# Performance work log

Measured on AMD Instinct MI355X. Metric: run time of the kernel, lower is better.

## Reference

```python
import jax, jax.numpy as jnp
import numpy as np

B, T, E, D = 4, 4096, 1024, 64

def setup_inputs() -> dict:
    key = jax.random.key(0)
    kx, kq, kk, kv = jax.random.split(key, 4)
    # kaiming_normal_ on [E, D] (fan_in = E in torch default mode='fan_in'):
    std = (2.0 / E) ** 0.5
    return {
        "x": jax.random.normal(kx, (B, T, E), dtype=jnp.float32),
        "Wq": jax.random.normal(kq, (E, D), dtype=jnp.float32) * std,
        "Wk": jax.random.normal(kk, (E, D), dtype=jnp.float32) * std,
        "Wv": jax.random.normal(kv, (E, D), dtype=jnp.float32) * std,
    }

def reference(x, Wq, Wk, Wv):
    q = jnp.einsum('bte,ei->bti', x, Wq)
    k = jnp.einsum('bte,ei->bti', x, Wk)
    v = jnp.einsum('bte,ei->bti', x, Wv)
    scale = 1.0 / jnp.sqrt(jnp.asarray(q.shape[-1], q.dtype))
    qk = jnp.einsum('bti,bTi->btT', q, k)  # [B, T, T] full score matrix
    s = jax.nn.softmax(qk * scale, axis=-1)
    return jnp.einsum('btT,bTi->bti', s, v)
```

## Files before the change

kernel.cpp:

```cpp
#include <hip/hip_runtime.h>
#include <stdint.h>


#define T_DIM 4096
#define E_DIM 1024
#define D_DIM 64
#define NROWS 16384

typedef __bf16 bf16x8 __attribute__((ext_vector_type(8)));
typedef float  f32x4  __attribute__((ext_vector_type(4)));

__global__ void conv_w(const float* __restrict__ Wq, const float* __restrict__ Wk,
                       const float* __restrict__ Wv, __bf16* __restrict__ wF)
{
    int idx = blockIdx.x * 256 + threadIdx.x;
    if (idx >= 196608) return;
    int j    = idx & 7;
    int lane = (idx >> 3) & 63;
    int n    = (idx >> 9) & 3;
    int ktG  = (idx >> 11) & 31;
    int m    = idx >> 16;
    int d = n * 16 + (lane & 15);
    int e = ktG * 32 + (lane >> 4) * 8 + j;
    const float* W = (m == 0) ? Wq : (m == 1) ? Wk : Wv;
    float v = W[e * D_DIM + d];
    if (m == 0) v *= 0.125f;
    wF[idx] = (__bf16)v;
}

__global__ __launch_bounds__(256) void aaaa_qkvpj(const float* __restrict__ x,
        const __bf16* __restrict__ wF,
        __bf16* __restrict__ Qp, __bf16* __restrict__ Kp, __bf16* __restrict__ Vt)
{
    __shared__ float red[12 * 16 * 66];

    const int tid  = threadIdx.x;
    const int lane = tid & 63;
    const int w    = tid >> 6;
    const int lrow = lane & 15;
    const int lq   = lane >> 4;
    const int r0   = blockIdx.x * 16;

    f32x4 acc[3][4] = {};
    const float* xrow = x + (long)(r0 + lrow) * E_DIM + w * 256;
    const __bf16* wl  = wF + lane * 8;

    #pragma unroll
    for (int kt = 0; kt < 8; ++kt) {
        const int k0 = kt * 32 + lq * 8;
        f32x4 xa = *(const f32x4*)(xrow + k0);
        f32x4 xb = *(const f32x4*)(xrow + k0 + 4);
        bf16x8 a;
        a[0] = (__bf16)xa[0]; a[1] = (__bf16)xa[1];
        a[2] = (__bf16)xa[2]; a[3] = (__bf16)xa[3];
        a[4] = (__bf16)xb[0]; a[5] = (__bf16)xb[1];
        a[6] = (__bf16)xb[2]; a[7] = (__bf16)xb[3];
        #pragma unroll
        for (int m = 0; m < 3; ++m) {
            #pragma unroll
            for (int n = 0; n < 4; ++n) {
                bf16x8 b = *(const bf16x8*)(wl + (((((m * 32) + (w * 8) + kt) * 4) + n) << 9));
                acc[m][n] = __builtin_amdgcn_mfma_f32_16x16x32_bf16(a, b, acc[m][n], 0, 0, 0);
            }
        }
    }

    #pragma unroll
    for (int m = 0; m < 3; ++m)
        #pragma unroll
        for (int n = 0; n < 4; ++n)
            #pragma unroll
            for (int j = 0; j < 4; ++j)
                red[((w * 3 + m) * 16 + lq * 4 + j) * 66 + n * 16 + lrow] = acc[m][n][j];
    __syncthreads();

    const long gb = r0 >> 12;
    const int  t0 = r0 & 4095;

    #pragma unroll
    for (int m = 0; m < 2; ++m)
        #pragma unroll
        for (int e = 0; e < 4; ++e) {
            int idx = e * 256 + tid;
            int r = idx >> 6, c = idx & 63;
            float s = red[(m * 16 + r) * 66 + c] + red[((3 + m) * 16 + r) * 66 + c]
                    + red[((6 + m) * 16 + r) * 66 + c] + red[((9 + m) * 16 + r) * 66 + c];
            (m == 0 ? Qp : Kp)[(long)(r0 + r) * D_DIM + c] = (__bf16)s;
        }
    #pragma unroll
    for (int e = 0; e < 4; ++e) {
        int idx = e * 256 + tid;
        int d = idx >> 4, tr = idx & 15;
        float s = red[(2 * 16 + tr) * 66 + d] + red[(5 * 16 + tr) * 66 + d]
                + red[(8 * 16 + tr) * 66 + d] + red[(11 * 16 + tr) * 66 + d];
        Vt[gb * (D_DIM * (long)T_DIM) + (long)d * T_DIM + t0 + tr] = (__bf16)s;
    }
}

#define PADK 72
__global__ __launch_bounds__(256) void flash_attn(const __bf16* __restrict__ Qp,
        const __bf16* __restrict__ Kp, const __bf16* __restrict__ Vt,
        float* __restrict__ Op, float* __restrict__ mp, float* __restrict__ lp,
        float* __restrict__ out, int ntile, int direct)
{
    __shared__ __bf16 kt[64][PADK];
    __shared__ __bf16 vt[64][PADK];
    __shared__ __bf16 pl[4][16][PADK];

    const int tid  = threadIdx.x;
    const int lane = tid & 63;
    const int w    = tid >> 6;
    const int lrow = lane & 15;
    const int lq   = lane >> 4;
    const int bid  = blockIdx.x;
    const int sp   = bid >> 8;
    const int rem  = bid & 255;
    const int b    = rem >> 6;
    const int qt   = rem & 63;
    const long base = (long)b * T_DIM;

    bf16x8 qf[2];
    {
        const __bf16* qptr = Qp + (base + qt * 64 + w * 16 + lrow) * D_DIM + lq * 8;
        qf[0] = *(const bf16x8*)(qptr);
        qf[1] = *(const bf16x8*)(qptr + 32);
    }

    f32x4 oacc[4] = {};
    float mrun[4], lrun[4];
    #pragma unroll
    for (int j = 0; j < 4; ++j) { mrun[j] = -1e30f; lrun[j] = 0.f; }

    const int ldrow = tid >> 2;
    const int ldcol = (tid & 3) * 16;
    const __bf16* vbase = Vt + b * (D_DIM * (long)T_DIM) + (long)ldrow * T_DIM;

    const int kv0 = sp * ntile;
    #pragma unroll 1
    for (int kv = kv0; kv < kv0 + ntile; ++kv) {
        __syncthreads();
        {
            const __bf16* kg = Kp + (base + kv * 64 + ldrow) * D_DIM + ldcol;
            const __bf16* vg = vbase + kv * 64 + ldcol;
            bf16x8 k0 = *(const bf16x8*)kg;
            bf16x8 k1 = *(const bf16x8*)(kg + 8);
            bf16x8 v0 = *(const bf16x8*)vg;
            bf16x8 v1 = *(const bf16x8*)(vg + 8);
            *(bf16x8*)&kt[ldrow][ldcol]     = k0;
            *(bf16x8*)&kt[ldrow][ldcol + 8] = k1;
            *(bf16x8*)&vt[ldrow][ldcol]     = v0;
            *(bf16x8*)&vt[ldrow][ldcol + 8] = v1;
        }
        __syncthreads();

        f32x4 sacc[4] = {};
        #pragma unroll
        for (int n = 0; n < 4; ++n)
            #pragma unroll
            for (int kk = 0; kk < 2; ++kk) {
                bf16x8 bk = *(const bf16x8*)&kt[n * 16 + lrow][kk * 32 + lq * 8];
                sacc[n] = __builtin_amdgcn_mfma_f32_16x16x32_bf16(qf[kk], bk, sacc[n], 0, 0, 0);
            }

        float pmax[4];
        #pragma unroll
        for (int j = 0; j < 4; ++j)
            pmax[j] = fmaxf(fmaxf(sacc[0][j], sacc[1][j]), fmaxf(sacc[2][j], sacc[3][j]));
        #pragma unroll
        for (int m = 1; m < 16; m <<= 1)
            #pragma unroll
            for (int j = 0; j < 4; ++j)
                pmax[j] = fmaxf(pmax[j], __shfl_xor(pmax[j], m));

        float p[4][4], alpha[4], rsum[4];
        #pragma unroll
        for (int j = 0; j < 4; ++j) {
            float mn = fmaxf(mrun[j], pmax[j]);
            alpha[j] = __expf(mrun[j] - mn);
            mrun[j]  = mn;
            float s = 0.f;
            #pragma unroll
            for (int n = 0; n < 4; ++n) { p[n][j] = __expf(sacc[n][j] - mn); s += p[n][j]; }
            rsum[j] = s;
        }
        #pragma unroll
        for (int m = 1; m < 16; m <<= 1)
            #pragma unroll
            for (int j = 0; j < 4; ++j)
                rsum[j] += __shfl_xor(rsum[j], m);
        #pragma unroll
        for (int j = 0; j < 4; ++j) lrun[j] = lrun[j] * alpha[j] + rsum[j];
        #pragma unroll
        for (int n = 0; n < 4; ++n)
            #pragma unroll
            for (int j = 0; j < 4; ++j)
                oacc[n][j] *= alpha[j];

        #pragma unroll
        for (int n = 0; n < 4; ++n)
            #pragma unroll
            for (int j = 0; j < 4; ++j)
                pl[w][lq * 4 + j][n * 16 + lrow] = (__bf16)p[n][j];

        #pragma unroll
        for (int kb = 0; kb < 2; ++kb) {
            bf16x8 pa = *(const bf16x8*)&pl[w][lrow][kb * 32 + lq * 8];
            #pragma unroll
            for (int n = 0; n < 4; ++n) {
                bf16x8 bv = *(const bf16x8*)&vt[n * 16 + lrow][kb * 32 + lq * 8];
                oacc[n] = __builtin_amdgcn_mfma_f32_16x16x32_bf16(pa, bv, oacc[n], 0, 0, 0);
            }
        }
    }

    if (direct) {
        #pragma unroll
        for (int j = 0; j < 4; ++j) {
            float inv = 1.0f / lrun[j];
            long row = base + qt * 64 + w * 16 + lq * 4 + j;
            #pragma unroll
            for (int n = 0; n < 4; ++n)
                out[row * D_DIM + n * 16 + lrow] = oacc[n][j] * inv;
        }
    } else {
        #pragma unroll
        for (int j = 0; j < 4; ++j) {
            int ro = w * 16 + lq * 4 + j;
            #pragma unroll
            for (int n = 0; n < 4; ++n)
                Op[((long)bid * 64 + ro) * D_DIM + n * 16 + lrow] = oacc[n][j];
            if (lrow == 0) {
                mp[bid * 64 + ro] = mrun[j];
                lp[bid * 64 + ro] = lrun[j];
            }
        }
    }
}

__global__ __launch_bounds__(256) void ab_combine(const float* __restrict__ Op,
        const float* __restrict__ mp, const float* __restrict__ lp,
        float* __restrict__ out, int nsplit)
{
    int idx = blockIdx.x * 256 + threadIdx.x;
    int d   = idx & 63;
    int row = idx >> 6;
    int b   = row >> 12;
    int t   = row & 4095;
    int qt  = t >> 6;
    int r   = t & 63;

    int pb0 = b * 64 + qt;
    float M = -1e30f;
    for (int s = 0; s < nsplit; ++s)
        M = fmaxf(M, mp[(s * 256 + pb0) * 64 + r]);
    float L = 0.f, O = 0.f;
    for (int s = 0; s < nsplit; ++s) {
        int pb = s * 256 + pb0;
        float wgt = __expf(mp[pb * 64 + r] - M);
        L += wgt * lp[pb * 64 + r];
        O += wgt * Op[((long)pb * 64 + r) * D_DIM + d];
    }
    out[idx] = O / L;
}

extern "C" void kernel_launch(void* const* d_in, const int* in_sizes, int n_in,
                              void* d_out, int out_size, void* d_ws, size_t ws_size,
                              hipStream_t stream)
{
    const float* x  = (const float*)d_in[0];
    const float* Wq = (const float*)d_in[1];
    const float* Wk = (const float*)d_in[2];
    const float* Wv = (const float*)d_in[3];
    float* out = (float*)d_out;

    char* wsb = (char*)d_ws;
    __bf16* wF = (__bf16*)wsb;
    __bf16* Qp = (__bf16*)(wsb + 524288);
    __bf16* Kp = (__bf16*)(wsb + 2621440);
    __bf16* Vt = (__bf16*)(wsb + 4718592);
    float*  mp = (float*)(wsb + 6815744);
    float*  lp = (float*)(wsb + 7340032);
    float*  Op = (float*)(wsb + 7864320);
    const size_t NEED8 = 7864320ull + 33554432ull;
    const size_t NEED4 = 7864320ull + 16777216ull;

    conv_w    <<<768, 256, 0, stream>>>(Wq, Wk, Wv, wF);
    aaaa_qkvpj<<<1024, 256, 0, stream>>>(x, wF, Qp, Kp, Vt);
    if (ws_size >= NEED8) {
        flash_attn<<<2048, 256, 0, stream>>>(Qp, Kp, Vt, Op, mp, lp, nullptr, 8, 0);
        ab_combine<<<4096, 256, 0, stream>>>(Op, mp, lp, out, 8);
    } else if (ws_size >= NEED4) {
        flash_attn<<<1024, 256, 0, stream>>>(Qp, Kp, Vt, Op, mp, lp, nullptr, 16, 0);
        ab_combine<<<4096, 256, 0, stream>>>(Op, mp, lp, out, 4);
    } else {
        flash_attn<<<256, 256, 0, stream>>>(Qp, Kp, Vt, nullptr, nullptr, nullptr, out, 64, 1);
    }
}
```

Baseline: 195.0 us.

## Pre-pack K/V into MFMA fragment layout and load directly to registers

Adds a repack kernel that stores K and V in the per-lane MFMA fragment order, so flash attention reads its B operands straight from global memory into registers. This removes the LDS staging and both __syncthreads per KV tile. Each wave now handles 32 query rows instead of 16, so every K/V fragment is reused across two row tiles, and the grid is halved. The combine kernel is templated on the split count to unroll its loops. The projection reduction buffer is switched to fp16 to cut shared memory, which costs an extra launch, extra workspace and some precision in the partial sums.

New measurement: 188.4 us. 3.4% less time.

```diff
diff --git a/kernel.cpp b/kernel.cpp
--- a/kernel.cpp
+++ b/kernel.cpp
@@ -32,7 +32,7 @@
         const __bf16* __restrict__ wF,
         __bf16* __restrict__ Qp, __bf16* __restrict__ Kp, __bf16* __restrict__ Vt)
 {
-    __shared__ float red[12 * 16 * 66];
+    __shared__ _Float16 red[12 * 16 * 66];
 
     const int tid  = threadIdx.x;
     const int lane = tid & 63;
@@ -71,7 +71,7 @@
         for (int n = 0; n < 4; ++n)
             #pragma unroll
             for (int j = 0; j < 4; ++j)
-                red[((w * 3 + m) * 16 + lq * 4 + j) * 66 + n * 16 + lrow] = acc[m][n][j];
+                red[((w * 3 + m) * 16 + lq * 4 + j) * 66 + n * 16 + lrow] = (_Float16)acc[m][n][j];
     __syncthreads();
 
     const long gb = r0 >> 12;
@@ -83,29 +83,48 @@
         for (int e = 0; e < 4; ++e) {
             int idx = e * 256 + tid;
             int r = idx >> 6, c = idx & 63;
-            float s = red[(m * 16 + r) * 66 + c] + red[((3 + m) * 16 + r) * 66 + c]
-                    + red[((6 + m) * 16 + r) * 66 + c] + red[((9 + m) * 16 + r) * 66 + c];
+            float s = (float)red[(m * 16 + r) * 66 + c] + (float)red[((3 + m) * 16 + r) * 66 + c]
+                    + (float)red[((6 + m) * 16 + r) * 66 + c] + (float)red[((9 + m) * 16 + r) * 66 + c];
             (m == 0 ? Qp : Kp)[(long)(r0 + r) * D_DIM + c] = (__bf16)s;
         }
     #pragma unroll
     for (int e = 0; e < 4; ++e) {
         int idx = e * 256 + tid;
         int d = idx >> 4, tr = idx & 15;
-        float s = red[(2 * 16 + tr) * 66 + d] + red[(5 * 16 + tr) * 66 + d]
-                + red[(8 * 16 + tr) * 66 + d] + red[(11 * 16 + tr) * 66 + d];
+        float s = (float)red[(2 * 16 + tr) * 66 + d] + (float)red[(5 * 16 + tr) * 66 + d]
+                + (float)red[(8 * 16 + tr) * 66 + d] + (float)red[(11 * 16 + tr) * 66 + d];
         Vt[gb * (D_DIM * (long)T_DIM) + (long)d * T_DIM + t0 + tr] = (__bf16)s;
     }
 }
 
-#define PADK 72
+__global__ __launch_bounds__(256) void aaab_rpack(const __bf16* __restrict__ Kp,
+        const __bf16* __restrict__ Vt, __bf16* __restrict__ KVf)
+{
+    int idx  = blockIdx.x * 256 + threadIdx.x;
+    int lane = idx & 63;
+    int frag = idx >> 6;
+    int isV  = frag >> 11;
+    int f    = frag & 2047;
+    int n    = f & 3;
+    int kh   = (f >> 2) & 1;
+    int kvt  = (f >> 3) & 63;
+    int b    = f >> 9;
+    bf16x8 v;
+    if (!isV)
+        v = *(const bf16x8*)&Kp[(long)(b * 4096 + kvt * 64 + n * 16 + (lane & 15)) * 64
+                                + kh * 32 + (lane >> 4) * 8];
+    else
+        v = *(const bf16x8*)&Vt[(long)(b * 64 + n * 16 + (lane & 15)) * 4096
+                                + kvt * 64 + kh * 32 + (lane >> 4) * 8];
+    *(bf16x8*)&KVf[(long)frag * 512 + lane * 8] = v;
+}
+
 __global__ __launch_bounds__(256) void flash_attn(const __bf16* __restrict__ Qp,
-        const __bf16* __restrict__ Kp, const __bf16* __restrict__ Vt,
+        const __bf16* __restrict__ KVf,
         float* __restrict__ Op, float* __restrict__ mp, float* __restrict__ lp,
         float* __restrict__ out, int ntile, int direct)
 {
-    __shared__ __bf16 kt[64][PADK];
-    __shared__ __bf16 vt[64][PADK];
-    __shared__ __bf16 pl[4][16][PADK];
+    __shared__ __bf16 pl[4][32][72];
 
     const int tid  = threadIdx.x;
     const int lane = tid & 63;
@@ -113,128 +132,160 @@
     const int lrow = lane & 15;
     const int lq   = lane >> 4;
     const int bid  = blockIdx.x;
-    const int sp   = bid >> 8;
-    const int rem  = bid & 255;
-    const int b    = rem >> 6;
-    const int qt   = rem & 63;
-    const long base = (long)b * T_DIM;
-
-    bf16x8 qf[2];
-    {
-        const __bf16* qptr = Qp + (base + qt * 64 + w * 16 + lrow) * D_DIM + lq * 8;
-        qf[0] = *(const bf16x8*)(qptr);
-        qf[1] = *(const bf16x8*)(qptr + 32);
-    }
-
-    f32x4 oacc[4] = {};
-    float mrun[4], lrun[4];
-    #pragma unroll
-    for (int j = 0; j < 4; ++j) { mrun[j] = -1e30f; lrun[j] = 0.f; }
-
-    const int ldrow = tid >> 2;
-    const int ldcol = (tid & 3) * 16;
-    const __bf16* vbase = Vt + b * (D_DIM * (long)T_DIM) + (long)ldrow * T_DIM;
+    const int sp   = bid >> 7;
+    const int qb   = bid & 127;
+    const int b    = qb >> 5;
+    const int qt   = qb & 31;
+    const int q0   = qt * 128 + w * 32;
+    const int grow0 = b * 4096 + q0;
+
+    bf16x8 qf[2][2];
+    #pragma unroll
+    for (int mi = 0; mi < 2; ++mi) {
+        const __bf16* qptr = Qp + (long)(grow0 + mi * 16 + lrow) * 64 + lq * 8;
+        qf[mi][0] = *(const bf16x8*)(qptr);
+        qf[mi][1] = *(const bf16x8*)(qptr + 32);
+    }
+
+    f32x4 oacc[2][4] = {};
+    float mrun[2][4], lrun[2][4];
+    #pragma unroll
+    for (int mi = 0; mi < 2; ++mi)
+        #pragma unroll
+        for (int j = 0; j < 4; ++j) { mrun[mi][j] = -1e30f; lrun[mi][j] = 0.f; }
+
+    const __bf16* kb_ = KVf + ((long)b * 512) * 512 + lane * 8;
+    const __bf16* vb_ = KVf + ((long)(2048 + b * 512)) * 512 + lane * 8;
 
     const int kv0 = sp * ntile;
     #pragma unroll 1
     for (int kv = kv0; kv < kv0 + ntile; ++kv) {
-        __syncthreads();
-        {
-            const __bf16* kg = Kp + (base + kv * 64 + ldrow) * D_DIM + ldcol;
-            const __bf16* vg = vbase + kv * 64 + ldcol;
-            bf16x8 k0 = *(const bf16x8*)kg;
-            bf16x8 k1 = *(const bf16x8*)(kg + 8);
-            bf16x8 v0 = *(const bf16x8*)vg;
-            bf16x8 v1 = *(const bf16x8*)(vg + 8);
-            *(bf16x8*)&kt[ldrow][ldcol]     = k0;
-            *(bf16x8*)&kt[ldrow][ldcol + 8] = k1;
-            *(bf16x8*)&vt[ldrow][ldcol]     = v0;
-            *(bf16x8*)&vt[ldrow][ldcol + 8] = v1;
+        const __bf16* kf = kb_ + (kv << 12);
+        const __bf16* vf = vb_ + (kv << 12);
+
+        bf16x8 kfr[2][4];
+        #pragma unroll
+        for (int kh = 0; kh < 2; ++kh)
+            #pragma unroll
+            for (int n = 0; n < 4; ++n)
+                kfr[kh][n] = *(const bf16x8*)(kf + ((kh * 4 + n) << 9));
+
+        f32x4 sacc[2][4] = {};
+        #pragma unroll
+        for (int mi = 0; mi < 2; ++mi)
+            #pragma unroll
+            for (int n = 0; n < 4; ++n)
+                #pragma unroll
+                for (int kh = 0; kh < 2; ++kh)
+                    sacc[mi][n] = __builtin_amdgcn_mfma_f32_16x16x32_bf16(
+                        qf[mi][kh], kfr[kh][n], sacc[mi][n], 0, 0, 0);
+
+        bf16x8 vfr[2][4];
+        #pragma unroll
+        for (int kh = 0; kh < 2; ++kh)
+            #pragma unroll
+            for (int n = 0; n < 4; ++n)
+                vfr[kh][n] = *(const bf16x8*)(vf + ((kh * 4 + n) << 9));
+
+        #pragma unroll
+        for (int mi = 0; mi < 2; ++mi) {
+            float pmax[4];
+            #pragma unroll
+            for (int j = 0; j < 4; ++j)
+                pmax[j] = fmaxf(fmaxf(sacc[mi][0][j], sacc[mi][1][j]),
+                                fmaxf(sacc[mi][2][j], sacc[mi][3][j]));
+            #pragma unroll
+            for (int m = 1; m < 16; m <<= 1)
+                #pragma unroll
+                for (int j = 0; j < 4; ++j)
+                    pmax[j] = fmaxf(pmax[j], __shfl_xor(pmax[j], m));
+
+            float rsum[4];
+            #pragma unroll
+            for (int j = 0; j < 4; ++j) {
+                float mn = fmaxf(mrun[mi][j], pmax[j]);
+                float alpha = __expf(mrun[mi][j] - mn);
+                mrun[mi][j] = mn;
+                float s = 0.f;
+                #pragma unroll
+                for (int n = 0; n < 4; ++n) {
+                    float pv = __expf(sacc[mi][n][j] - mn);
+                    s += pv;
+                    pl[w][mi * 16 + lq * 4 + j][n * 16 + lrow] = (__bf16)pv;
+                }
+                rsum[j] = s;
+                #pragma unroll
+                for (int n = 0; n < 4; ++n)
+                    oacc[mi][n][j] *= alpha;
+                lrun[mi][j] *= alpha;
+            }
+            #pragma unroll
+            for (int m = 1; m < 16; m <<= 1)
+                #pragma unroll
+                for (int j = 0; j < 4; ++j)
+                    rsum[j] += __shfl_xor(rsum[j], m);
+            #pragma unroll
+            for (int j = 0; j < 4; ++j) lrun[mi][j] += rsum[j];
         }
-        __syncthreads();
-
-        f32x4 sacc[4] = {};
-        #pragma unroll
-        for (int n = 0; n < 4; ++n)
-            #pragma unroll
-            for (int kk = 0; kk < 2; ++kk) {
-                bf16x8 bk = *(const bf16x8*)&kt[n * 16 + lrow][kk * 32 + lq * 8];
-                sacc[n] = __builtin_amdgcn_mfma_f32_16x16x32_bf16(qf[kk], bk, sacc[n], 0, 0, 0);
-            }
-
-        float pmax[4];
-        #pragma unroll
-        for (int j = 0; j < 4; ++j)
-            pmax[j] = fmaxf(fmaxf(sacc[0][j], sacc[1][j]), fmaxf(sacc[2][j], sacc[3][j]));
-        #pragma unroll
-        for (int m = 1; m < 16; m <<= 1)
-            #pragma unroll
-            for (int j = 0; j < 4; ++j)
-                pmax[j] = fmaxf(pmax[j], __shfl_xor(pmax[j], m));
-
-        float p[4][4], alpha[4], rsum[4];
-        #pragma unroll
-        for (int j = 0; j < 4; ++j) {
-            float mn = fmaxf(mrun[j], pmax[j]);
-            alpha[j] = __expf(mrun[j] - mn);
-            mrun[j]  = mn;
-            float s = 0.f;
-            #pragma unroll
-            for (int n = 0; n < 4; ++n) { p[n][j] = __expf(sacc[n][j] - mn); s += p[n][j]; }
-            rsum[j] = s;
-        }
-        #pragma unroll
-        for (int m = 1; m < 16; m <<= 1)
-            #pragma unroll
-            for (int j = 0; j < 4; ++j)
-                rsum[j] += __shfl_xor(rsum[j], m);
-        #pragma unroll
-        for (int j = 0; j < 4; ++j) lrun[j] = lrun[j] * alpha[j] + rsum[j];
-        #pragma unroll
-        for (int n = 0; n < 4; ++n)
-            #pragma unroll
-            for (int j = 0; j < 4; ++j)
-                oacc[n][j] *= alpha[j];
-
-        #pragma unroll
-        for (int n = 0; n < 4; ++n)
-            #pragma unroll
-            for (int j = 0; j < 4; ++j)
-                pl[w][lq * 4 + j][n * 16 + lrow] = (__bf16)p[n][j];
-
-        #pragma unroll
-        for (int kb = 0; kb < 2; ++kb) {
-            bf16x8 pa = *(const bf16x8*)&pl[w][lrow][kb * 32 + lq * 8];
-            #pragma unroll
-            for (int n = 0; n < 4; ++n) {
-                bf16x8 bv = *(const bf16x8*)&vt[n * 16 + lrow][kb * 32 + lq * 8];
-                oacc[n] = __builtin_amdgcn_mfma_f32_16x16x32_bf16(pa, bv, oacc[n], 0, 0, 0);
-            }
-        }
+
+        #pragma unroll
+        for (int mi = 0; mi < 2; ++mi)
+            #pragma unroll
+            for (int kh = 0; kh < 2; ++kh) {
+                bf16x8 pa = *(const bf16x8*)&pl[w][mi * 16 + lrow][kh * 32 + lq * 8];
+                #pragma unroll
+                for (int n = 0; n < 4; ++n)
+                    oacc[mi][n] = __builtin_amdgcn_mfma_f32_16x16x32_bf16(
+                        pa, vfr[kh][n], oacc[mi][n], 0, 0, 0);
+            }
     }
 
     if (direct) {
         #pragma unroll
-        for (int j = 0; j < 4; ++j) {
-            float inv = 1.0f / lrun[j];
-            long row = base + qt * 64 + w * 16 + lq * 4 + j;
-            #pragma unroll
-            for (int n = 0; n < 4; ++n)
-                out[row * D_DIM + n * 16 + lrow] = oacc[n][j] * inv;
-        }
+        for (int mi = 0; mi < 2; ++mi)
+            #pragma unroll
+            for (int j = 0; j < 4; ++j) {
+                float inv = 1.0f / lrun[mi][j];
+                long row = grow0 + mi * 16 + lq * 4 + j;
+                #pragma unroll
+                for (int n = 0; n < 4; ++n)
+                    out[row * 64 + n * 16 + lrow] = oacc[mi][n][j] * inv;
+            }
     } else {
         #pragma unroll
-        for (int j = 0; j < 4; ++j) {
-            int ro = w * 16 + lq * 4 + j;
-            #pragma unroll
-            for (int n = 0; n < 4; ++n)
-                Op[((long)bid * 64 + ro) * D_DIM + n * 16 + lrow] = oacc[n][j];
-            if (lrow == 0) {
-                mp[bid * 64 + ro] = mrun[j];
-                lp[bid * 64 + ro] = lrun[j];
-            }
-        }
-    }
+        for (int mi = 0; mi < 2; ++mi)
+            #pragma unroll
+            for (int j = 0; j < 4; ++j) {
+                long prow = (long)sp * NROWS + grow0 + mi * 16 + lq * 4 + j;
+                #pragma unroll
+                for (int n = 0; n < 4; ++n)
+                    Op[prow * 64 + n * 16 + lrow] = oacc[mi][n][j];
+                if (lrow == 0) {
+                    mp[prow] = mrun[mi][j];
+                    lp[prow] = lrun[mi][j];
+                }
+            }
+    }
+}
+
+template <int NS>
+__device__ __forceinline__ void combine_body(const float* Op, const float* mp,
+        const float* lp, float* out, int idx)
+{
+    int d    = idx & 63;
+    int grow = idx >> 6;
+    float M = -1e30f;
+    float ms[NS];
+    #pragma unroll
+    for (int s = 0; s < NS; ++s) { ms[s] = mp[s * NROWS + grow]; M = fmaxf(M, ms[s]); }
+    float L = 0.f, O = 0.f;
+    #pragma unroll
+    for (int s = 0; s < NS; ++s) {
+        float wgt = __expf(ms[s] - M);
+        L += wgt * lp[s * NROWS + grow];
+        O += wgt * Op[((long)s * NROWS + grow) * 64 + d];
+    }
+    out[idx] = O / L;
 }
 
 __global__ __launch_bounds__(256) void ab_combine(const float* __restrict__ Op,
@@ -242,25 +293,8 @@
         float* __restrict__ out, int nsplit)
 {
     int idx = blockIdx.x * 256 + threadIdx.x;
-    int d   = idx & 63;
-    int row = idx >> 6;
-    int b   = row >> 12;
-    int t   = row & 4095;
-    int qt  = t >> 6;
-    int r   = t & 63;
-
-    int pb0 = b * 64 + qt;
-    float M = -1e30f;
-    for (int s = 0; s < nsplit; ++s)
-        M = fmaxf(M, mp[(s * 256 + pb0) * 64 + r]);
-    float L = 0.f, O = 0.f;
-    for (int s = 0; s < nsplit; ++s) {
-        int pb = s * 256 + pb0;
-        float wgt = __expf(mp[pb * 64 + r] - M);
-        L += wgt * lp[pb * 64 + r];
-        O += wgt * Op[((long)pb * 64 + r) * D_DIM + d];
-    }
-    out[idx] = O / L;
+    if (nsplit == 8) combine_body<8>(Op, mp, lp, out, idx);
+    else             combine_body<4>(Op, mp, lp, out, idx);
 }
 
 extern "C" void kernel_launch(void* const* d_in, const int* in_sizes, int n_in,
@@ -274,25 +308,27 @@
     float* out = (float*)d_out;
 
     char* wsb = (char*)d_ws;
-    __bf16* wF = (__bf16*)wsb;
-    __bf16* Qp = (__bf16*)(wsb + 524288);
-    __bf16* Kp = (__bf16*)(wsb + 2621440);
-    __bf16* Vt = (__bf16*)(wsb + 4718592);
-    float*  mp = (float*)(wsb + 6815744);
-    float*  lp = (float*)(wsb + 7340032);
-    float*  Op = (float*)(wsb + 7864320);
-    const size_t NEED8 = 7864320ull + 33554432ull;
-    const size_t NEED4 = 7864320ull + 16777216ull;
+    __bf16* wF  = (__bf16*)wsb;
+    __bf16* Qp  = (__bf16*)(wsb + 524288);
+    __bf16* Kp  = (__bf16*)(wsb + 2621440);
+    __bf16* Vt  = (__bf16*)(wsb + 4718592);
+    __bf16* KVf = (__bf16*)(wsb + 6815744);
+    float*  mp  = (float*)(wsb + 11010048);
+    float*  lp  = (float*)(wsb + 11534336);
+    float*  Op  = (float*)(wsb + 12058624);
+    const size_t NEED8 = 12058624ull + 33554432ull;
+    const size_t NEED4 = 12058624ull + 16777216ull;
 
     conv_w    <<<768, 256, 0, stream>>>(Wq, Wk, Wv, wF);
     aaaa_qkvpj<<<1024, 256, 0, stream>>>(x, wF, Qp, Kp, Vt);
+    aaab_rpack<<<1024, 256, 0, stream>>>(Kp, Vt, KVf);
     if (ws_size >= NEED8) {
-        flash_attn<<<2048, 256, 0, stream>>>(Qp, Kp, Vt, Op, mp, lp, nullptr, 8, 0);
+        flash_attn<<<1024, 256, 0, stream>>>(Qp, KVf, Op, mp, lp, nullptr, 8, 0);
         ab_combine<<<4096, 256, 0, stream>>>(Op, mp, lp, out, 8);
     } else if (ws_size >= NEED4) {
-        flash_attn<<<1024, 256, 0, stream>>>(Qp, Kp, Vt, Op, mp, lp, nullptr, 16, 0);
+        flash_attn<<<512, 256, 0, stream>>>(Qp, KVf, Op, mp, lp, nullptr, 16, 0);
         ab_combine<<<4096, 256, 0, stream>>>(Op, mp, lp, out, 4);
     } else {
-        flash_attn<<<256, 256, 0, stream>>>(Qp, Kp, Vt, nullptr, nullptr, nullptr, out, 64, 1);
-    }
-}
+        flash_attn<<<128, 256, 0, stream>>>(Qp, KVf, nullptr, nullptr, nullptr, out, 64, 1);
+    }
+}
```
